# Optimization experiments

Measured on AMD Instinct MI355X. Metric: run time of the kernel, lower is better.

Reference implementation:

```python
import jax, jax.numpy as jnp
import numpy as np
from jax import lax

A_RATIOS = (0.5, 1.0, 2.0)
A_SCALES = (8, 16, 32)
FEAT_STRIDE = 16
BASE_SIZE = 16
PRE_NMS = 6000     # n_test_pre_nms
POST_NMS = 300     # n_test_post_nms
NMS_THRESH = 0.7
MIN_SIZE = 16.0
SCALE = 1.0        # forward(scale=1.0) default
NEG = -1e10


def _anchor_base():
    # standard generate_anchor_base: centered at (8,8), ratios x scales
    py = px = BASE_SIZE / 2.0
    rows = []
    for r in A_RATIOS:
        for s in A_SCALES:
            h = BASE_SIZE * s * np.sqrt(r)
            w = BASE_SIZE * s * np.sqrt(1.0 / r)
            rows.append([py - h / 2.0, px - w / 2.0, py + h / 2.0, px + w / 2.0])
    return np.asarray(rows, np.float32)  # (A, 4)


def _all_anchors(height, width):
    base = jnp.asarray(_anchor_base())                                  # (A, 4)
    sy = (jnp.arange(height) * FEAT_STRIDE).astype(jnp.float32)
    sx = (jnp.arange(width) * FEAT_STRIDE).astype(jnp.float32)
    gy, gx = jnp.meshgrid(sy, sx, indexing='ij')
    shift = jnp.stack([gy.ravel(), gx.ravel(), gy.ravel(), gx.ravel()], axis=1)  # (K, 4)
    anch = base[None, :, :] + shift[:, None, :]                         # (K, A, 4)
    return anch.reshape(-1, 4)                                          # (K*A, 4)


def _conv(x, w, b, pad):
    y = lax.conv_general_dilated(x, w, (1, 1), [(pad, pad), (pad, pad)],
                                 dimension_numbers=('NCHW', 'OIHW', 'NCHW'))
    return y + b[None, :, None, None]


def _loc2bbox(anchors, locs):
    h = anchors[:, 2] - anchors[:, 0]
    w = anchors[:, 3] - anchors[:, 1]
    cy = anchors[:, 0] + 0.5 * h
    cx = anchors[:, 1] + 0.5 * w
    dy, dx, dh, dw = locs[:, 0], locs[:, 1], locs[:, 2], locs[:, 3]
    ncy = dy * h + cy
    ncx = dx * w + cx
    nh = jnp.exp(dh) * h
    nw = jnp.exp(dw) * w
    return jnp.stack([ncy - 0.5 * nh, ncx - 0.5 * nw,
                      ncy + 0.5 * nh, ncx + 0.5 * nw], axis=1)


def _iou_one_vs_all(box, boxes):
    ty = jnp.maximum(box[0], boxes[:, 0])
    tx = jnp.maximum(box[1], boxes[:, 1])
    by = jnp.minimum(box[2], boxes[:, 2])
    bx = jnp.minimum(box[3], boxes[:, 3])
    inter = jnp.maximum(by - ty, 0.0) * jnp.maximum(bx - tx, 0.0)
    a1 = (box[2] - box[0]) * (box[3] - box[1])
    a2 = (boxes[:, 2] - boxes[:, 0]) * (boxes[:, 3] - boxes[:, 1])
    return inter / (a1 + a2 - inter + 1e-9)


def _nms(boxes, scores):
    # greedy NMS with fixed POST_NMS output; invalid slots are zero boxes
    def step(s, _):
        i = jnp.argmax(s)
        valid = s[i] > NEG / 2
        ious = _iou_one_vs_all(boxes[i], boxes)
        s = jnp.where(ious > NMS_THRESH, NEG, s)  # suppresses self (iou=1)
        return s, (i, valid)
    _, (idx, valid) = lax.scan(step, scores, None, length=POST_NMS)
    return boxes[idx] * valid[:, None].astype(boxes.dtype)  # (POST_NMS, 4)


def _proposals(anchors, locs, fg, img_h, img_w):
    boxes = _loc2bbox(anchors, locs)
    boxes = jnp.stack([jnp.clip(boxes[:, 0], 0.0, img_h),
                       jnp.clip(boxes[:, 1], 0.0, img_w),
                       jnp.clip(boxes[:, 2], 0.0, img_h),
                       jnp.clip(boxes[:, 3], 0.0, img_w)], axis=1)
    hs = boxes[:, 2] - boxes[:, 0]
    ws = boxes[:, 3] - boxes[:, 1]
    ok = (hs >= MIN_SIZE * SCALE) & (ws >= MIN_SIZE * SCALE)
    sc = jnp.where(ok, fg, NEG)
    top_sc, idx = lax.top_k(sc, PRE_NMS)
    return _nms(boxes[idx], top_sc)


def reference(base_feat, W_conv1, b_conv1, W_score, b_score, W_loc, b_loc, img_h, img_w):
    N, _, H, W = base_feat.shape
    A = 9
    mid = jax.nn.relu(_conv(base_feat, W_conv1, b_conv1, 1))            # (N,512,H,W)
    rpn_locs = _conv(mid, W_loc, b_loc, 0).transpose(0, 2, 3, 1).reshape(N, H * W * A, 4)
    raw = _conv(mid, W_score, b_score, 0).transpose(0, 2, 3, 1)          # (N,H,W,2A)
    rpn_scores = raw.reshape(N, H * W * A, 2)
    fg = jax.nn.softmax(raw.reshape(N, H, W, A, 2), axis=-1)[..., 1].reshape(N, -1)
    anchors = _all_anchors(H, W)                                         # (H*W*A,4)
    ih, iw = float(img_h), float(img_w)
    prop = jax.vmap(lambda l, f: _proposals(anchors, l, f, ih, iw))(rpn_locs, fg)
    rois = prop.reshape(N * POST_NMS, 4)
    roi_indices = jnp.repeat(jnp.arange(N, dtype=jnp.int32), POST_NMS)
    return rpn_locs, rpn_scores, rois, roi_indices, anchors


def setup_inputs() -> dict:
    key = jax.random.key(0)
    k0, k1, k2, k3 = jax.random.split(key, 4)
    N, C, H, W = 4, 512, 64, 64
    nA = 9
    return {
        'base_feat': jax.random.normal(k0, (N, C, H, W), jnp.float32),
        'W_conv1': 0.01 * jax.random.normal(k1, (512, 512, 3, 3), jnp.float32),
        'b_conv1': jnp.zeros((512,), jnp.float32),
        'W_score': 0.01 * jax.random.normal(k2, (2 * nA, 512, 1, 1), jnp.float32),
        'b_score': jnp.zeros((2 * nA,), jnp.float32),
        'W_loc': 0.01 * jax.random.normal(k3, (4 * nA, 512, 1, 1), jnp.float32),
        'b_loc': jnp.zeros((4 * nA,), jnp.float32),
        'img_h': 1024,
        'img_w': 1024,
    }
```

## Files before the change

### kernel.cpp

```cpp
#include <hip/hip_runtime.h>
#include <math.h>

#define HH 64
#define WW 64
#define NIMG 4
#define CIN 512
#define AA 9
#define HWA (HH*WW*AA)
#define PRE_NMS 6000
#define POST_NMS 300
#define NEGV (-1e10f)
#define NEGK 0xD01502F9u
#define NWORD 94

#define OFF1 589824
#define OFF2 884736
#define OFF3 889536
#define OFF4 890736

typedef unsigned int u32;
typedef unsigned long long u64;
typedef _Float16 f16;
typedef _Float16 half8 __attribute__((ext_vector_type(8)));
typedef float f32x4 __attribute__((ext_vector_type(4)));

__device__ __forceinline__ void gload_lds16(const void* g, void* l)
{
    __builtin_amdgcn_global_load_lds((const __attribute__((address_space(1))) void*)g,
                                     (__attribute__((address_space(3))) void*)l,
                                     16, 0, 0);
}

__global__ __launch_bounds__(256) void k_prep_x(const float* __restrict__ x,
                                                f16* __restrict__ xh,
                                                f16* __restrict__ xl)
{
    __shared__ float tile[64][65];
    int ci0 = blockIdx.x * 64, y = blockIdx.y, n = blockIdx.z;
    int t = threadIdx.x;
    #pragma unroll
    for (int l = 0; l < 16; ++l) {
        int idx = l * 256 + t;
        int cc = idx >> 6, xc = idx & 63;
        tile[cc][xc] = x[((size_t)(n * CIN + ci0 + cc) * HH + y) * WW + xc];
    }
    __syncthreads();
    #pragma unroll
    for (int l = 0; l < 16; ++l) {
        int idx = l * 256 + t;
        int xc = idx >> 6, cc = idx & 63;
        float v = tile[cc][xc];
        f16 hi = (f16)v;
        f16 lo = (f16)(v - (float)hi);
        size_t o = ((size_t)(n * 64 + y) * 64 + xc) * 512 + ci0 + cc;
        xh[o] = hi; xl[o] = lo;
    }
}

__global__ __launch_bounds__(256) void k_prep_w(const float* __restrict__ W1,
                                                f16* __restrict__ wh,
                                                f16* __restrict__ wl)
{
    int idx = blockIdx.x * 256 + threadIdx.x;
    int co = idx >> 9, ci = idx & 511;
    #pragma unroll
    for (int tap = 0; tap < 9; ++tap) {
        float v = W1[(size_t)idx * 9 + tap];
        f16 hi = (f16)v;
        f16 lo = (f16)(v - (float)hi);
        size_t o = ((size_t)tap * 512 + co) * 512 + ci;
        wh[o] = hi; wl[o] = lo;
    }
}

__global__ __launch_bounds__(256, 4) void k_conv_mfma(const f16* __restrict__ xh,
                                                      const f16* __restrict__ xl,
                                                      const f16* __restrict__ wh,
                                                      const f16* __restrict__ wl,
                                                      const float* __restrict__ bias,
                                                      float* __restrict__ mid)
{
    __shared__ f16 sX[2][4][64][32];
    const int t = threadIdx.x;
    const int co0 = blockIdx.x * 64, yb = blockIdx.y, n = blockIdx.z;
    const int y0 = yb * 2;
    const int wv = t >> 6, lane = t & 63;
    const int q = lane >> 4, li = lane & 15;
    const int mh = wv & 1;
    const int xhp = wv >> 1;

    if (yb == 0 || yb == 31) {
        int rowu = (yb == 0) ? 0 : 3072;
        u32* p = (u32*)&sX[0][0][0][0];
        #pragma unroll
        for (int l = 0; l < 8; ++l) {
            int idx = l * 256 + t;
            int plane = idx >> 10, r = idx & 1023;
            p[plane * 4096 + rowu + r] = 0;
        }
    }

    f32x4 acc[2][2][2];
    #pragma unroll
    for (int mt = 0; mt < 2; ++mt)
        #pragma unroll
        for (int xn = 0; xn < 2; ++xn)
            #pragma unroll
            for (int yy = 0; yy < 2; ++yy)
                acc[mt][xn][yy] = (f32x4){0.f, 0.f, 0.f, 0.f};

    auto prefetch = [&](int ci0) {
        #pragma unroll
        for (int m = 0; m < 8; ++m) {
            int k2 = wv * 8 + m;
            int plane = k2 >> 4;
            int row = (k2 >> 2) & 3;
            int gy = y0 - 1 + row;
            if ((unsigned)gy < 64u) {
                int col = ((k2 & 3) << 4) + (lane >> 2);
                int s = (lane & 3) ^ ((lane >> 3) & 3);
                const f16* src = (plane ? xl : xh) +
                    (((size_t)(n * 64 + gy) * 64 + col) * 512 + ci0 + s * 8);
                f16* dst = &sX[0][0][0][0] + (size_t)k2 * 512 + lane * 8;
                gload_lds16(src, dst);
            }
        }
    };

    half8 wa[2][2], wn[2][2];
    auto loadW = [&](half8 w[2][2], int ci0, int tap) {
        #pragma unroll
        for (int mt = 0; mt < 2; ++mt) {
            size_t base = ((size_t)(tap * 512) + co0 + mh * 32 + mt * 16 + li) * 512 + ci0 + q * 8;
            w[0][mt] = *(const half8*)(wh + base);
            w[1][mt] = *(const half8*)(wl + base);
        }
    };

    prefetch(0);
    loadW(wa, 0, 0);

    const half8 zero8 = {(f16)0, (f16)0, (f16)0, (f16)0, (f16)0, (f16)0, (f16)0, (f16)0};

    for (int chunk = 0; chunk < 16; ++chunk) {
        const int ci0 = chunk * 32;
        __syncthreads();

        #pragma unroll
        for (int tap = 0; tap < 9; ++tap) {
            if (tap < 8) loadW(wn, ci0, tap + 1);
            const int ky = tap / 3, kx = tap - ky * 3;

            half8 B[2][2][2];
            #pragma unroll
            for (int xn = 0; xn < 2; ++xn) {
                int xc = xhp * 32 + xn * 16 + li;
                int colr = xc + kx - 1;
                bool oob = (colr < 0) || (colr > 63);
                int colc = oob ? 0 : colr;
                int qe = q ^ ((colc >> 1) & 3);
                #pragma unroll
                for (int yy = 0; yy < 2; ++yy) {
                    int row = yy + ky;
                    const f16* ph = &sX[0][row][colc][qe * 8];
                    half8 vh = *(const half8*)ph;
                    half8 vl = *(const half8*)(ph + 8192);
                    if (oob) { vh = zero8; vl = zero8; }
                    B[0][xn][yy] = vh; B[1][xn][yy] = vl;
                }
            }
            #pragma unroll
            for (int mt = 0; mt < 2; ++mt)
                #pragma unroll
                for (int xn = 0; xn < 2; ++xn)
                    #pragma unroll
                    for (int yy = 0; yy < 2; ++yy)
                        acc[mt][xn][yy] = __builtin_amdgcn_mfma_f32_16x16x32_f16(wa[0][mt], B[0][xn][yy], acc[mt][xn][yy], 0, 0, 0);
            #pragma unroll
            for (int mt = 0; mt < 2; ++mt)
                #pragma unroll
                for (int xn = 0; xn < 2; ++xn)
                    #pragma unroll
                    for (int yy = 0; yy < 2; ++yy)
                        acc[mt][xn][yy] = __builtin_amdgcn_mfma_f32_16x16x32_f16(wa[0][mt], B[1][xn][yy], acc[mt][xn][yy], 0, 0, 0);
            #pragma unroll
            for (int mt = 0; mt < 2; ++mt)
                #pragma unroll
                for (int xn = 0; xn < 2; ++xn)
                    #pragma unroll
                    for (int yy = 0; yy < 2; ++yy)
                        acc[mt][xn][yy] = __builtin_amdgcn_mfma_f32_16x16x32_f16(wa[1][mt], B[0][xn][yy], acc[mt][xn][yy], 0, 0, 0);

            if (tap < 8) {
                #pragma unroll
                for (int pl = 0; pl < 2; ++pl)
                    #pragma unroll
                    for (int mt = 0; mt < 2; ++mt) wa[pl][mt] = wn[pl][mt];
            }
        }

        if (chunk + 1 < 16) {
            __syncthreads();
            prefetch(ci0 + 32);
            loadW(wa, ci0 + 32, 0);
        }
    }

    #pragma unroll
    for (int mt = 0; mt < 2; ++mt) {
        #pragma unroll
        for (int r = 0; r < 4; ++r) {
            int co = co0 + mh * 32 + mt * 16 + q * 4 + r;
            float bv = bias[co];
            #pragma unroll
            for (int xn = 0; xn < 2; ++xn) {
                int xc = xhp * 32 + xn * 16 + li;
                #pragma unroll
                for (int yy = 0; yy < 2; ++yy) {
                    float v = acc[mt][xn][yy][r] + bv;
                    mid[((size_t)(n * 512 + co) * HH + y0 + yy) * WW + xc] = v > 0.f ? v : 0.f;
                }
            }
        }
    }
}

__global__ __launch_bounds__(256) void k_htrans(const float* __restrict__ Ws,
                                                const float* __restrict__ Wl,
                                                float* __restrict__ Wt2)
{
    int i = blockIdx.x * 256 + threadIdx.x;
    if (i >= 512 * 64) return;
    int ci = i >> 6, co = i & 63;
    float v = 0.f;
    if (co < 18) v = Ws[co * 512 + ci];
    else if (co < 54) v = Wl[(co - 18) * 512 + ci];
    Wt2[i] = v;
}

__global__ __launch_bounds__(256) void k_hgemm(const float* __restrict__ mid,
                                               const float* __restrict__ Wt2,
                                               float* __restrict__ sraw)
{
    __shared__ float sM[32][64];
    __shared__ float sW2[32][64];
    const int t = threadIdx.x;
    const int px0 = blockIdx.x * 64, n = blockIdx.y;
    const int tx = t & 15, ty = t >> 4;

    float acc[4][4];
    #pragma unroll
    for (int c = 0; c < 4; ++c)
        #pragma unroll
        for (int j = 0; j < 4; ++j) acc[c][j] = 0.f;

    for (int ci0 = 0; ci0 < 512; ci0 += 32) {
        __syncthreads();
        #pragma unroll
        for (int l = 0; l < 8; ++l) {
            int i = l * 256 + t;
            int ci = i >> 6, px = i & 63;
            sM[ci][px] = mid[((size_t)n * 512 + ci0 + ci) * 4096 + px0 + px];
            sW2[ci][px] = Wt2[(size_t)(ci0 + ci) * 64 + px];
        }
        __syncthreads();
        #pragma unroll
        for (int ci = 0; ci < 32; ++ci) {
            float mv[4], wv[4];
            #pragma unroll
            for (int j = 0; j < 4; ++j) mv[j] = sM[ci][tx * 4 + j];
            #pragma unroll
            for (int c = 0; c < 4; ++c) wv[c] = sW2[ci][ty * 4 + c];
            #pragma unroll
            for (int c = 0; c < 4; ++c)
                #pragma unroll
                for (int j = 0; j < 4; ++j) acc[c][j] += wv[c] * mv[j];
        }
    }
    #pragma unroll
    for (int c = 0; c < 4; ++c) {
        float4 v = make_float4(acc[c][0], acc[c][1], acc[c][2], acc[c][3]);
        *(float4*)&sraw[((size_t)n * 64 + ty * 4 + c) * 4096 + px0 + tx * 4] = v;
    }
}

__global__ __launch_bounds__(256) void k_decode(const float* __restrict__ sraw,
                                                const float* __restrict__ bsc,
                                                const float* __restrict__ blc,
                                                const int* __restrict__ ph,
                                                const int* __restrict__ pw,
                                                float* __restrict__ out,
                                                float* __restrict__ boxes,
                                                u32* __restrict__ key)
{
    int p = blockIdx.x * 256 + threadIdx.x;
    int n = p >> 12, pi = p & 4095;
    int y = pi >> 6, xq = pi & 63;

    const float* S = sraw + (size_t)n * 64 * 4096 + pi;
    float* o0 = out + (size_t)n * 147456;
    float* o1 = out + OFF1 + (size_t)n * 73728;
    float IHf = (float)(*ph), IWf = (float)(*pw);

    #pragma unroll
    for (int a = 0; a < 9; ++a) {
        float s0 = S[(size_t)(2 * a) * 4096] + bsc[2 * a];
        float s1 = S[(size_t)(2 * a + 1) * 4096] + bsc[2 * a + 1];
        float dy = S[(size_t)(18 + 4 * a) * 4096] + blc[4 * a];
        float dx = S[(size_t)(19 + 4 * a) * 4096] + blc[4 * a + 1];
        float dh = S[(size_t)(20 + 4 * a) * 4096] + blc[4 * a + 2];
        float dw = S[(size_t)(21 + 4 * a) * 4096] + blc[4 * a + 3];

        o1[(pi * 9 + a) * 2 + 0] = s0;
        o1[(pi * 9 + a) * 2 + 1] = s1;
        o0[(pi * 9 + a) * 4 + 0] = dy;
        o0[(pi * 9 + a) * 4 + 1] = dx;
        o0[(pi * 9 + a) * 4 + 2] = dh;
        o0[(pi * 9 + a) * 4 + 3] = dw;

        float mm = fmaxf(s0, s1);
        float e0 = expf(s0 - mm), e1 = expf(s1 - mm);
        float fg = e1 / (e0 + e1);

        int ri = a / 3, si = a - ri * 3;
        double s = (double)(8 << si);
        double rr = (ri == 0) ? 0.5 : ((ri == 1) ? 1.0 : 2.0);
        double hh = 16.0 * s * sqrt(rr);
        double wd = 16.0 * s * sqrt(1.0 / rr);
        float a0 = (float)(8.0 - hh * 0.5) + (float)(y * 16);
        float a1 = (float)(8.0 - wd * 0.5) + (float)(xq * 16);
        float a2 = (float)(8.0 + hh * 0.5) + (float)(y * 16);
        float a3 = (float)(8.0 + wd * 0.5) + (float)(xq * 16);

        float h = a2 - a0, w = a3 - a1;
        float cy = a0 + 0.5f * h, cx = a1 + 0.5f * w;
        float ncy = dy * h + cy, ncx = dx * w + cx;
        float nh = expf(dh) * h, nw = expf(dw) * w;
        float b0 = fminf(fmaxf(ncy - 0.5f * nh, 0.f), IHf);
        float b1 = fminf(fmaxf(ncx - 0.5f * nw, 0.f), IWf);
        float b2 = fminf(fmaxf(ncy + 0.5f * nh, 0.f), IHf);
        float b3 = fminf(fmaxf(ncx + 0.5f * nw, 0.f), IWf);

        bool ok = (b2 - b0 >= 16.0f) && (b3 - b1 >= 16.0f);
        float sc = ok ? fg : NEGV;

        int gi = n * HWA + pi * 9 + a;
        ((float4*)boxes)[gi] = make_float4(b0, b1, b2, b3);
        u32 u = __float_as_uint(sc);
        u32 kasc = (u & 0x80000000u) ? ~u : (u | 0x80000000u);
        key[gi] = ~kasc;
    }
}

__global__ void k_misc(float* __restrict__ out)
{
    int i = blockIdx.x * 256 + threadIdx.x;
    if (i < 4800) out[OFF2 + i] = 0.f;
    if (i < 1200) out[OFF3 + i] = (float)(i / 300);
    if (i < HWA) {
        int pi = i / 9, a = i - pi * 9;
        int y = pi >> 6, xq = pi & 63;
        int ri = a / 3, si = a - ri * 3;
        double s = (double)(8 << si);
        double rr = (ri == 0) ? 0.5 : ((ri == 1) ? 1.0 : 2.0);
        double hh = 16.0 * s * sqrt(rr);
        double wd = 16.0 * s * sqrt(1.0 / rr);
        out[OFF4 + i * 4 + 0] = (float)(8.0 - hh * 0.5) + (float)(y * 16);
        out[OFF4 + i * 4 + 1] = (float)(8.0 - wd * 0.5) + (float)(xq * 16);
        out[OFF4 + i * 4 + 2] = (float)(8.0 + hh * 0.5) + (float)(y * 16);
        out[OFF4 + i * 4 + 3] = (float)(8.0 + wd * 0.5) + (float)(xq * 16);
    }
}

__global__ __launch_bounds__(1024) void k_select(const u32* __restrict__ key,
                                                 u64* __restrict__ cmp,
                                                 int* __restrict__ nvalid)
{
    __shared__ int hist[256];
    __shared__ u32 sPref;
    __shared__ int sR;
    __shared__ int cLess, cEq, cVal;
    int n = blockIdx.x, t = threadIdx.x;
    const u32* k0 = key + (size_t)n * HWA;

    u32 pref = 0, mask = 0;
    int R = PRE_NMS;
    for (int pass = 0; pass < 4; ++pass) {
        int shift = 24 - pass * 8;
        if (t < 256) hist[t] = 0;
        __syncthreads();
        for (int i = t; i < HWA; i += 1024) {
            u32 k = k0[i];
            if ((k & mask) == pref) atomicAdd(&hist[(k >> shift) & 255], 1);
        }
        __syncthreads();
        if (t == 0) {
            int cum = 0;
            for (int b = 0; b < 256; ++b) {
                int c = hist[b];
                if (cum + c >= R) { sPref = pref | ((u32)b << shift); sR = R - cum; break; }
                cum += c;
            }
        }
        __syncthreads();
        pref = sPref; R = sR; mask |= (0xFFu << shift);
        __syncthreads();
    }
    u32 T = pref;
    if (t == 0) { cLess = 0; cEq = 0; cVal = 0; }
    __syncthreads();
    for (int i = t; i < HWA; i += 1024) {
        u32 k = k0[i];
        if (k < NEGK) atomicAdd(&cVal, 1);
        if (k < T) {
            int p = atomicAdd(&cLess, 1);
            cmp[(size_t)n * 8192 + p] = ((u64)k << 32) | (u32)i;
        } else if (k == T) {
            int p = atomicAdd(&cEq, 1);
            if (p < R) cmp[(size_t)n * 8192 + (PRE_NMS - 1 - p)] = ((u64)k << 32) | (u32)i;
        }
    }
    for (int i = PRE_NMS + t; i < 8192; i += 1024) cmp[(size_t)n * 8192 + i] = ~0ull;
    __syncthreads();
    if (t == 0) nvalid[n] = cVal < PRE_NMS ? cVal : PRE_NMS;
}

__global__ __launch_bounds__(1024) void k_sort(const u64* __restrict__ cmp,
                                               const float* __restrict__ boxes,
                                               float* __restrict__ boxesS)
{
    __shared__ u64 sK[8192];
    int n = blockIdx.x, t = threadIdx.x;
    for (int i = t; i < 8192; i += 1024) sK[i] = cmp[(size_t)n * 8192 + i];
    for (unsigned k = 2; k <= 8192; k <<= 1) {
        for (unsigned j = k >> 1; j > 0; j >>= 1) {
            __syncthreads();
            #pragma unroll
            for (int v = 0; v < 8; ++v) {
                int i = v * 1024 + t;
                int ixj = i ^ (int)j;
                if (ixj > i) {
                    u64 a = sK[i], b = sK[ixj];
                    bool up = ((i & (int)k) == 0);
                    if (up ? (a > b) : (a < b)) { sK[i] = b; sK[ixj] = a; }
                }
            }
        }
    }
    __syncthreads();
    const float4* bsrc = (const float4*)boxes + (size_t)n * HWA;
    float4* bdst = (float4*)boxesS + (size_t)n * PRE_NMS;
    for (int i = t; i < PRE_NMS; i += 1024) {
        u32 idx = (u32)(sK[i] & 0xFFFFFFFFu);
        bdst[i] = bsrc[idx];
    }
}

__global__ __launch_bounds__(64) void k_iou(const float* __restrict__ boxesS,
                                            u64* __restrict__ mask)
{
    __shared__ float4 cb[64];
    int w = blockIdx.x, ic = blockIdx.y, n = blockIdx.z;
    if (w < ic) return;
    int t = threadIdx.x;
    const float4* B = (const float4*)boxesS + (size_t)n * PRE_NMS;
    int jc = w * 64 + t;
    cb[t] = (jc < PRE_NMS) ? B[jc] : make_float4(0.f, 0.f, 0.f, 0.f);
    __syncthreads();
    int i = ic * 64 + t;
    if (i >= PRE_NMS) return;
    float4 bb = B[i];
    float area1 = (bb.z - bb.x) * (bb.w - bb.y);
    u64 m = 0;
    #pragma unroll 8
    for (int j = 0; j < 64; ++j) {
        float4 o = cb[j];
        float ty_ = fmaxf(bb.x, o.x), tx_ = fmaxf(bb.y, o.y);
        float by_ = fminf(bb.z, o.z), bx_ = fminf(bb.w, o.w);
        float inter = fmaxf(by_ - ty_, 0.f) * fmaxf(bx_ - tx_, 0.f);
        float area2 = (o.z - o.x) * (o.w - o.y);
        float iou = inter / (area1 + area2 - inter + 1e-9f);
        if (iou > 0.7f) m |= (1ull << j);
    }
    mask[((size_t)n * PRE_NMS + i) * NWORD + w] = m;
}

__global__ __launch_bounds__(64) void k_nms3(const u64* __restrict__ mask,
                                             const int* __restrict__ nvalid,
                                             const float* __restrict__ boxesS,
                                             float* __restrict__ rois)
{
    int n = blockIdx.x, lane = threadIdx.x;
    int nv = nvalid[n];
    const u64* M = mask + (size_t)n * PRE_NMS * NWORD;
    const float4* B = (const float4*)boxesS + (size_t)n * PRE_NMS;

    auto vmask = [&](int w) -> u64 {
        int lo = w * 64;
        if (nv >= lo + 64) return ~0ull;
        if (nv <= lo) return 0ull;
        return (1ull << (nv - lo)) - 1ull;
    };
    u64 vm0 = vmask(lane);
    u64 vm1 = (lane < NWORD - 64) ? vmask(64 + lane) : 0ull;
    u64 rem0 = 0, rem1 = 0;

    int cnt = 0;
    while (cnt < POST_NMS) {
        u64 c0 = (~rem0) & vm0;
        u64 c1 = (~rem1) & vm1;
        int sel;
        u64 b0 = __ballot(c0 != 0);
        if (b0) {
            int l = __builtin_ctzll(b0);
            u64 w = __shfl(c0, l);
            sel = l * 64 + __builtin_ctzll(w);
        } else {
            u64 b1 = __ballot(c1 != 0);
            if (!b1) break;
            int l = __builtin_ctzll(b1);
            u64 w = __shfl(c1, l);
            sel = (64 + l) * 64 + __builtin_ctzll(w);
        }
        if (lane == 0) {
            float4 bb = B[sel];
            float* orow = rois + (size_t)(n * POST_NMS + cnt) * 4;
            orow[0] = bb.x; orow[1] = bb.y; orow[2] = bb.z; orow[3] = bb.w;
        }
        const u64* Mr = M + (size_t)sel * NWORD;
        rem0 |= Mr[lane];
        if (lane < NWORD - 64) rem1 |= Mr[64 + lane];
        cnt++;
    }
}

extern "C" void kernel_launch(void* const* d_in, const int* in_sizes, int n_in,
                              void* d_out, int out_size, void* d_ws, size_t ws_size,
                              hipStream_t stream)
{
    const float* x  = (const float*)d_in[0];
    const float* W1 = (const float*)d_in[1];
    const float* b1 = (const float*)d_in[2];
    const float* Ws = (const float*)d_in[3];
    const float* bs = (const float*)d_in[4];
    const float* Wl = (const float*)d_in[5];
    const float* bl = (const float*)d_in[6];
    const int* ih   = (const int*)d_in[7];
    const int* iw   = (const int*)d_in[8];
    float* out = (float*)d_out;
    char* ws = (char*)d_ws;

    f16*   Wh2    = (f16*)  (ws);
    f16*   Wl2    = (f16*)  (ws + 4718592);
    float* mid    = (float*)(ws + 9437184);
    f16*   xh     = (f16*)  (ws + 42991616);
    f16*   xl     = (f16*)  (ws + 59768832);
    float* boxes  = (float*)(ws + 42991616);
    u32*   key    = (u32*)  (ws + 45350912);
    u64*   cmp    = (u64*)  (ws + 45940736);
    float* boxesS = (float*)(ws + 46202880);
    int*   nval   = (int*)  (ws + 46586880);
    float* Wt2    = (float*)(ws);
    float* sraw   = (float*)(ws + 262144);
    u64*   iomask = (u64*)  (ws + 9437184);

    k_prep_x<<<dim3(8, 64, 4), 256, 0, stream>>>(x, xh, xl);
    k_prep_w<<<1024, 256, 0, stream>>>(W1, Wh2, Wl2);
    k_conv_mfma<<<dim3(8, 32, 4), 256, 0, stream>>>(xh, xl, Wh2, Wl2, b1, mid);
    k_htrans<<<128, 256, 0, stream>>>(Ws, Wl, Wt2);
    k_hgemm<<<dim3(64, 4), 256, 0, stream>>>(mid, Wt2, sraw);
    k_decode<<<64, 256, 0, stream>>>(sraw, bs, bl, ih, iw, out, boxes, key);
    k_misc<<<144, 256, 0, stream>>>(out);
    k_select<<<4, 1024, 0, stream>>>(key, cmp, nval);
    k_sort<<<4, 1024, 0, stream>>>(cmp, boxes, boxesS);
    k_iou<<<dim3(NWORD, NWORD, NIMG), 64, 0, stream>>>(boxesS, iomask);
    k_nms3<<<NIMG, 64, 0, stream>>>(iomask, nval, boxesS, out + OFF2);
}
```

Before: 863.4 us.

## Double-buffer LDS B fragments across taps and remap blocks for L2 reuse

After: 846.9 us. Within noise of the previous version (-1.9%).

```diff
diff --git a/kernel.cpp b/kernel.cpp
--- a/kernel.cpp
+++ b/kernel.cpp
@@ -82,7 +82,11 @@
 {
     __shared__ f16 sX[2][4][64][32];
     const int t = threadIdx.x;
-    const int co0 = blockIdx.x * 64, yb = blockIdx.y, n = blockIdx.z;
+    const int lid = blockIdx.x + 8 * (blockIdx.y + 32 * blockIdx.z);
+    const int logical = (lid & 7) * 128 + (lid >> 3);
+    const int co0 = (logical & 7) * 64;
+    const int g = logical >> 3;
+    const int yb = g & 31, n = g >> 5;
     const int y0 = yb * 2;
     const int wv = t >> 6, lane = t & 63;
     const int q = lane >> 4, li = lane & 15;
@@ -127,47 +131,67 @@
         }
     };
 
+    const size_t wb0 = (size_t)(co0 + mh * 32 + li) * 512 + q * 8;
+    const f16* pWh = wh + wb0;
+    const f16* pWl = wl + wb0;
     half8 wa[2][2], wn[2][2];
-    auto loadW = [&](half8 w[2][2], int ci0, int tap) {
+    auto loadW = [&](half8 (&w)[2][2], int ci0, int tap) {
         #pragma unroll
         for (int mt = 0; mt < 2; ++mt) {
-            size_t base = ((size_t)(tap * 512) + co0 + mh * 32 + mt * 16 + li) * 512 + ci0 + q * 8;
-            w[0][mt] = *(const half8*)(wh + base);
-            w[1][mt] = *(const half8*)(wl + base);
+            size_t off = (size_t)tap * 262144 + (size_t)mt * 8192 + ci0;
+            w[0][mt] = *(const half8*)(pWh + off);
+            w[1][mt] = *(const half8*)(pWl + off);
+        }
+    };
+
+    const f16* pB[2][3];
+    bool ob[2][3];
+    #pragma unroll
+    for (int xn = 0; xn < 2; ++xn)
+        #pragma unroll
+        for (int kx = 0; kx < 3; ++kx) {
+            int xc = xhp * 32 + xn * 16 + li;
+            int colr = xc + kx - 1;
+            bool o = (colr < 0) || (colr > 63);
+            int colc = o ? 0 : colr;
+            int qe = q ^ ((colc >> 1) & 3);
+            ob[xn][kx] = o;
+            pB[xn][kx] = &sX[0][0][colc][qe * 8];
+        }
+
+    const half8 zero8 = {(f16)0, (f16)0, (f16)0, (f16)0, (f16)0, (f16)0, (f16)0, (f16)0};
+
+    auto loadB = [&](half8 (&Bf)[2][2][2], int tap) {
+        const int ky = tap / 3, kx = tap - ky * 3;
+        #pragma unroll
+        for (int xn = 0; xn < 2; ++xn) {
+            const f16* pb = pB[xn][kx];
+            #pragma unroll
+            for (int yy = 0; yy < 2; ++yy) {
+                const f16* ph = pb + (yy + ky) * 2048;
+                half8 vh = *(const half8*)ph;
+                half8 vl = *(const half8*)(ph + 8192);
+                if (ob[xn][kx]) { vh = zero8; vl = zero8; }
+                Bf[0][xn][yy] = vh; Bf[1][xn][yy] = vl;
+            }
         }
     };
 
     prefetch(0);
     loadW(wa, 0, 0);
-
-    const half8 zero8 = {(f16)0, (f16)0, (f16)0, (f16)0, (f16)0, (f16)0, (f16)0, (f16)0};
 
     for (int chunk = 0; chunk < 16; ++chunk) {
         const int ci0 = chunk * 32;
         __syncthreads();
 
+        half8 B0[2][2][2], Bn[2][2][2];
+        loadB(B0, 0);
+
         #pragma unroll
         for (int tap = 0; tap < 9; ++tap) {
-            if (tap < 8) loadW(wn, ci0, tap + 1);
-            const int ky = tap / 3, kx = tap - ky * 3;
-
-            half8 B[2][2][2];
-            #pragma unroll
-            for (int xn = 0; xn < 2; ++xn) {
-                int xc = xhp * 32 + xn * 16 + li;
-                int colr = xc + kx - 1;
-                bool oob = (colr < 0) || (colr > 63);
-                int colc = oob ? 0 : colr;
-                int qe = q ^ ((colc >> 1) & 3);
-                #pragma unroll
-                for (int yy = 0; yy < 2; ++yy) {
-                    int row = yy + ky;
-                    const f16* ph = &sX[0][row][colc][qe * 8];
-                    half8 vh = *(const half8*)ph;
-                    half8 vl = *(const half8*)(ph + 8192);
-                    if (oob) { vh = zero8; vl = zero8; }
-                    B[0][xn][yy] = vh; B[1][xn][yy] = vl;
-                }
+            if (tap < 8) {
+                loadW(wn, ci0, tap + 1);
+                loadB(Bn, tap + 1);
             }
             #pragma unroll
             for (int mt = 0; mt < 2; ++mt)
@@ -175,27 +199,33 @@
                 for (int xn = 0; xn < 2; ++xn)
                     #pragma unroll
                     for (int yy = 0; yy < 2; ++yy)
-                        acc[mt][xn][yy] = __builtin_amdgcn_mfma_f32_16x16x32_f16(wa[0][mt], B[0][xn][yy], acc[mt][xn][yy], 0, 0, 0);
+                        acc[mt][xn][yy] = __builtin_amdgcn_mfma_f32_16x16x32_f16(wa[0][mt], B0[0][xn][yy], acc[mt][xn][yy], 0, 0, 0);
             #pragma unroll
             for (int mt = 0; mt < 2; ++mt)
                 #pragma unroll
                 for (int xn = 0; xn < 2; ++xn)
                     #pragma unroll
                     for (int yy = 0; yy < 2; ++yy)
-                        acc[mt][xn][yy] = __builtin_amdgcn_mfma_f32_16x16x32_f16(wa[0][mt], B[1][xn][yy], acc[mt][xn][yy], 0, 0, 0);
+                        acc[mt][xn][yy] = __builtin_amdgcn_mfma_f32_16x16x32_f16(wa[0][mt], B0[1][xn][yy], acc[mt][xn][yy], 0, 0, 0);
             #pragma unroll
             for (int mt = 0; mt < 2; ++mt)
                 #pragma unroll
                 for (int xn = 0; xn < 2; ++xn)
                     #pragma unroll
                     for (int yy = 0; yy < 2; ++yy)
-                        acc[mt][xn][yy] = __builtin_amdgcn_mfma_f32_16x16x32_f16(wa[1][mt], B[0][xn][yy], acc[mt][xn][yy], 0, 0, 0);
+                        acc[mt][xn][yy] = __builtin_amdgcn_mfma_f32_16x16x32_f16(wa[1][mt], B0[0][xn][yy], acc[mt][xn][yy], 0, 0, 0);
 
             if (tap < 8) {
                 #pragma unroll
                 for (int pl = 0; pl < 2; ++pl)
                     #pragma unroll
                     for (int mt = 0; mt < 2; ++mt) wa[pl][mt] = wn[pl][mt];
+                #pragma unroll
+                for (int pl = 0; pl < 2; ++pl)
+                    #pragma unroll
+                    for (int xn = 0; xn < 2; ++xn)
+                        #pragma unroll
+                        for (int yy = 0; yy < 2; ++yy) B0[pl][xn][yy] = Bn[pl][xn][yy];
             }
         }
 
```
